# Kernel optimization log

Hardware: AMD Instinct MI355X
Metric: run time of the kernel (lower is better)

The kernel has to match this reference:

```python
import jax, jax.numpy as jnp
import numpy as np

N_NODES = 50000
N_EDGES = 640000
H_DIM = 128


def setup_inputs() -> dict:
    key = jax.random.key(0)
    k1, k2, k3, k4 = jax.random.split(key, 4)
    node_feat = jax.random.normal(k1, (N_NODES, H_DIM), dtype=jnp.float32)
    src = jax.random.randint(k2, (N_EDGES,), 0, N_NODES, dtype=jnp.int64)
    dst = jax.random.randint(k3, (N_EDGES,), 0, N_NODES, dtype=jnp.int64)
    # glorot-uniform kernel, zero bias (as in the original initializers)
    limit = np.sqrt(6.0 / (2 * H_DIM + H_DIM)).astype(np.float32)
    W = jax.random.uniform(k4, (2 * H_DIM, H_DIM), minval=-limit, maxval=limit, dtype=jnp.float32)
    b = jnp.zeros((H_DIM,), dtype=jnp.float32)
    return {"node_feat": node_feat, "src": src, "dst": dst, "W": W, "b": b}


def reference(node_feat, src, dst, W, b):
    # per-edge message: concat(h[src], h[dst]) -> linear  : [E, 2d] @ [2d, d]
    msg = jnp.concatenate([node_feat[src], node_feat[dst]], axis=-1)
    edge_feat = msg @ W + b  # [E, d]
    # scatter-sum over destination nodes (zero for in-degree-0 nodes, as DGL update_all)
    agg = jax.ops.segment_sum(edge_feat, dst, num_segments=node_feat.shape[0])  # [N, d]
    # node apply: sigmoid(aggregated msg) + softplus(old h)
    return jax.nn.sigmoid(agg) + jax.nn.softplus(node_feat)
```

## Files before the change

### kernel.cpp

```cpp
#include <hip/hip_runtime.h>
#include <math.h>

#define HD 128
#define CAP 32
#define OVCAP 8192
#define NPROD 256
#define PBCAP 64
#define BINSZ 512
#define MAXBINS 112
#define NPB 16
#define RPT 8

typedef __attribute__((ext_vector_type(8))) short bf16x8;
typedef __attribute__((ext_vector_type(4))) float f32x4;

__device__ inline short f2bf(float x) {
    union { float f; unsigned u; } v; v.f = x;
    unsigned r = v.u + 0x7fff + ((v.u >> 16) & 1);
    return (short)(r >> 16);
}

#define LOG2E 1.4426950408889634f
#define LN2   0.6931471805599453f

__device__ inline float fast_sigmoid(float x) {
    return __builtin_amdgcn_rcpf(1.0f + __builtin_amdgcn_exp2f(-LOG2E * x));
}
__device__ inline float fast_softplus(float x) {
    float t = __builtin_amdgcn_exp2f(-LOG2E * fabsf(x));
    return fmaxf(x, 0.0f) + LN2 * __builtin_amdgcn_logf(1.0f + t);
}

__device__ inline void accum8(float* a, const uint4 u) {
    a[0] += __uint_as_float(u.x << 16);
    a[1] += __uint_as_float(u.x & 0xffff0000u);
    a[2] += __uint_as_float(u.y << 16);
    a[3] += __uint_as_float(u.y & 0xffff0000u);
    a[4] += __uint_as_float(u.z << 16);
    a[5] += __uint_as_float(u.z & 0xffff0000u);
    a[6] += __uint_as_float(u.w << 16);
    a[7] += __uint_as_float(u.w & 0xffff0000u);
}


__global__ __launch_bounds__(256) void prep0(
    const float* __restrict__ W, short* __restrict__ WtG,
    int* __restrict__ ovA_cnt, int* __restrict__ ovB_cnt)
{
    const int tid = blockIdx.x * 256 + threadIdx.x;
    const int total = gridDim.x * 256;
    if (tid == 0) { *ovA_cnt = 0; *ovB_cnt = 0; }
    for (int i = tid; i < 256 * 128; i += total) {
        int j = i >> 7, k = i & 127;
        float w = (j < HD) ? W[k * HD + j] : W[(HD + k) * HD + (j - HD)];
        WtG[i] = f2bf(w);
    }
}

__global__ __launch_bounds__(256) void partA(
    const int* __restrict__ src, const int* __restrict__ dst,
    unsigned* __restrict__ pb_buf,
    int* __restrict__ pb_cnt,
    unsigned* __restrict__ ovA, int* __restrict__ ovA_cnt,
    int n_edges, int nbins)
{
    __shared__ unsigned buf[MAXBINS][PBCAP];
    __shared__ int bcnt[MAXBINS];

    const int t = threadIdx.x;
    for (int i = t; i < nbins; i += 256) bcnt[i] = 0;
    __syncthreads();

    const int chunk = (n_edges + NPROD - 1) / NPROD;
    int e0 = blockIdx.x * chunk;
    int e1 = e0 + chunk; if (e1 > n_edges) e1 = n_edges;

    for (int e = e0 + t; e < e1; e += 256) {
        int d = dst[e], s = src[e];
        int bin = d >> 9;
        unsigned pk = ((unsigned)d << 16) | (unsigned)s;
        int pos = atomicAdd(&bcnt[bin], 1);
        if (pos < PBCAP) buf[bin][pos] = pk;
        else {
            int op = atomicAdd(ovA_cnt, 1);
            if (op < OVCAP) ovA[op] = pk;
        }
    }
    __syncthreads();

    unsigned* myb = pb_buf + (size_t)blockIdx.x * nbins * PBCAP;
    int* myc = pb_cnt + (size_t)blockIdx.x * nbins;
    for (int b = 0; b < nbins; ++b) {
        int c = bcnt[b]; if (c > PBCAP) c = PBCAP;
        if (t < c) myb[(size_t)b * PBCAP + t] = buf[b][t];
        if (t == 0) myc[b] = c;
    }
}

__global__ __launch_bounds__(256) void partB(
    const unsigned* __restrict__ pb_buf, const int* __restrict__ pb_cnt,
    const unsigned* __restrict__ ovA, const int* __restrict__ ovA_cnt,
    unsigned* __restrict__ ovB, int* __restrict__ ovB_cnt,
    int* __restrict__ cnt, unsigned short* __restrict__ bkt,
    int n_nodes, int nbins)
{
    __shared__ unsigned short lbkt[BINSZ][CAP];
    __shared__ int lcnt[BINSZ];

    const int t = threadIdx.x;
    const int bin = blockIdx.x;
    const int base = bin * BINSZ;

    for (int i = t; i < BINSZ; i += 256) lcnt[i] = 0;
    __syncthreads();

    {
        int c = pb_cnt[(size_t)t * nbins + bin];
        const unsigned* seg = pb_buf + ((size_t)t * nbins + bin) * PBCAP;
        for (int i = 0; i < c; ++i) {
            unsigned e = seg[i];
            int dl = (int)(e >> 16) - base;
            int pos = atomicAdd(&lcnt[dl], 1);
            if (pos < CAP) lbkt[dl][pos] = (unsigned short)(e & 0xffffu);
            else {
                int op = atomicAdd(ovB_cnt, 1);
                if (op < OVCAP) ovB[op] = e;
            }
        }
    }
    {
        int oc = *ovA_cnt; if (oc > OVCAP) oc = OVCAP;
        for (int i = t; i < oc; i += 256) {
            unsigned e = ovA[i];
            int d = (int)(e >> 16);
            if ((d >> 9) == bin) {
                int dl = d - base;
                int pos = atomicAdd(&lcnt[dl], 1);
                if (pos < CAP) lbkt[dl][pos] = (unsigned short)(e & 0xffffu);
                else {
                    int op = atomicAdd(ovB_cnt, 1);
                    if (op < OVCAP) ovB[op] = e;
                }
            }
        }
    }
    __syncthreads();

    for (int g0 = t; g0 < BINSZ; g0 += 256) {
        int g = base + g0;
        if (g < n_nodes) {
            cnt[g] = lcnt[g0];
            uint4* dstp = (uint4*)(bkt + (size_t)g * CAP);
            const uint4* srcp = (const uint4*)&lbkt[g0][0];
            dstp[0] = srcp[0];
            dstp[1] = srcp[1];
            dstp[2] = srcp[2];
            dstp[3] = srcp[3];
        }
    }
}


__global__ __launch_bounds__(256) void prep_gemm(
    const float* __restrict__ h,
    const short* __restrict__ WtG,
    const float* __restrict__ bias,
    short* __restrict__ m1b,
    short* __restrict__ m2b,
    int n_nodes)
{
    __shared__ short sb[2][2][16][72];

    const int lane = threadIdx.x & 63;
    const int wv = threadIdx.x >> 6;
    const int half = wv & 1;
    const int ch = wv >> 1;
    const int c0 = ch * 64;
    const int row = lane & 15;
    const int g = lane >> 4;
    const int mBlk = blockIdx.x * 64;

    bf16x8 B[4][4];
    #pragma unroll
    for (int jt = 0; jt < 4; ++jt) {
        const short* wj = WtG + (size_t)(half * HD + c0 + jt * 16 + row) * HD + g * 8;
        #pragma unroll
        for (int kf = 0; kf < 4; ++kf)
            B[jt][kf] = *(const bf16x8*)(wj + kf * 32);
    }
    float bc[4];
    #pragma unroll
    for (int jt = 0; jt < 4; ++jt) bc[jt] = half ? bias[c0 + jt * 16 + row] : 0.f;

    short* const dstp = half ? m2b : m1b;

    float4 af[8];
    {
        int mA = mBlk + row; if (mA > n_nodes - 1) mA = n_nodes - 1;
        #pragma unroll
        for (int kf = 0; kf < 4; ++kf) {
            af[2 * kf]     = *(const float4*)(h + (size_t)mA * HD + kf * 32 + g * 8);
            af[2 * kf + 1] = *(const float4*)(h + (size_t)mA * HD + kf * 32 + g * 8 + 4);
        }
    }

    #pragma unroll
    for (int tt = 0; tt < 4; ++tt) {
        const int m0 = mBlk + tt * 16;

        bf16x8 a[4];
        #pragma unroll
        for (int kf = 0; kf < 4; ++kf) {
            float4 x = af[2 * kf], y = af[2 * kf + 1];
            bf16x8 t = { f2bf(x.x), f2bf(x.y), f2bf(x.z), f2bf(x.w),
                         f2bf(y.x), f2bf(y.y), f2bf(y.z), f2bf(y.w) };
            a[kf] = t;
        }
        if (tt < 3) {
            int mN = m0 + 16 + row; if (mN > n_nodes - 1) mN = n_nodes - 1;
            #pragma unroll
            for (int kf = 0; kf < 4; ++kf) {
                af[2 * kf]     = *(const float4*)(h + (size_t)mN * HD + kf * 32 + g * 8);
                af[2 * kf + 1] = *(const float4*)(h + (size_t)mN * HD + kf * 32 + g * 8 + 4);
            }
        }

        f32x4 acc[4];
        #pragma unroll
        for (int jt = 0; jt < 4; ++jt) acc[jt] = (f32x4){0.f, 0.f, 0.f, 0.f};
        #pragma unroll
        for (int jt = 0; jt < 4; ++jt)
            #pragma unroll
            for (int kf = 0; kf < 4; ++kf)
                acc[jt] = __builtin_amdgcn_mfma_f32_16x16x32_bf16(a[kf], B[jt][kf], acc[jt], 0, 0, 0);

        #pragma unroll
        for (int jt = 0; jt < 4; ++jt)
            #pragma unroll
            for (int r = 0; r < 4; ++r)
                sb[half][ch][g * 4 + r][jt * 16 + row] = f2bf(acc[jt][r] + bc[jt]);
        asm volatile("s_waitcnt lgkmcnt(0)" ::: "memory");
        #pragma unroll
        for (int ps = 0; ps < 2; ++ps) {
            int rr = ps * 8 + (lane >> 3);
            int c8 = lane & 7;
            int n = m0 + rr;
            bf16x8 v = *(const bf16x8*)&sb[half][ch][rr][c8 * 8];
            if (n < n_nodes)
                *(bf16x8*)(dstp + (size_t)n * HD + c0 + c8 * 8) = v;
        }
    }
}


__global__ __launch_bounds__(256) void gather_ep(
    const short* __restrict__ m1b, const int* __restrict__ cnt,
    const unsigned short* __restrict__ bkt,
    const unsigned* __restrict__ ov, const int* __restrict__ ov_cnt,
    const short* __restrict__ m2b,
    const float* __restrict__ h, float* __restrict__ out, int n_nodes)
{
    int g = (blockIdx.x * 256 + threadIdx.x) >> 4;
    int lane = threadIdx.x & 15;
    if (g >= n_nodes) return;
    const int degree = cnt[g];
    const int end = (degree < CAP) ? degree : CAP;
    const unsigned short* bl = bkt + (size_t)g * CAP;
    const size_t lo = (size_t)(lane * 8);

    float a0[8], a1[8];
    #pragma unroll
    for (int q = 0; q < 8; ++q) { a0[q] = 0.f; a1[q] = 0.f; }

    if (end > 0) {
        const int lastv = bl[end - 1];
        const uint4* bl4 = (const uint4*)bl;
        for (int base = 0; base < end; base += 8) {
            uint4 iv = bl4[base >> 3];
            int id8[8];
            id8[0] = iv.x & 0xffff; id8[1] = iv.x >> 16;
            id8[2] = iv.y & 0xffff; id8[3] = iv.y >> 16;
            id8[4] = iv.z & 0xffff; id8[5] = iv.z >> 16;
            id8[6] = iv.w & 0xffff; id8[7] = iv.w >> 16;
            #pragma unroll
            for (int j = 0; j < 8; ++j)
                if (base + j >= end) id8[j] = lastv;
            uint4 v[8];
            #pragma unroll
            for (int j = 0; j < 8; ++j)
                v[j] = *(const uint4*)(m1b + (size_t)id8[j] * HD + lo);
            #pragma unroll
            for (int j = 0; j < 8; ++j) {
                if (base + j < end) accum8((j & 1) ? a1 : a0, v[j]);
            }
        }
    }

    if (degree > CAP) {
        int oc = *ov_cnt; if (oc > OVCAP) oc = OVCAP;
        for (int i = 0; i < oc; ++i) {
            unsigned v = ov[i];
            if ((int)(v >> 16) == g) {
                uint4 vv = *(const uint4*)(m1b + (size_t)(v & 0xffffu) * HD + lo);
                accum8(a0, vv);
            }
        }
    }

    const float dg = (float)degree;
    uint4 mv = *(const uint4*)(m2b + (size_t)g * HD + lo);
    float mr[8];
    mr[0] = __uint_as_float(mv.x << 16); mr[1] = __uint_as_float(mv.x & 0xffff0000u);
    mr[2] = __uint_as_float(mv.y << 16); mr[3] = __uint_as_float(mv.y & 0xffff0000u);
    mr[4] = __uint_as_float(mv.z << 16); mr[5] = __uint_as_float(mv.z & 0xffff0000u);
    mr[6] = __uint_as_float(mv.w << 16); mr[7] = __uint_as_float(mv.w & 0xffff0000u);

    const float4* ph = (const float4*)(h + (size_t)g * HD + lo);
    float4 ha = ph[0], hb4 = ph[1];
    float hr[8] = { ha.x, ha.y, ha.z, ha.w, hb4.x, hb4.y, hb4.z, hb4.w };

    float o[8];
    #pragma unroll
    for (int q = 0; q < 8; ++q) {
        float agg = (a0[q] + a1[q]) + dg * mr[q];
        o[q] = fast_sigmoid(agg) + fast_softplus(hr[q]);
    }
    float4* po = (float4*)(out + (size_t)g * HD + lo);
    po[0] = (float4){o[0], o[1], o[2], o[3]};
    po[1] = (float4){o[4], o[5], o[6], o[7]};
}


__global__ __launch_bounds__(256) void zero_i32(int* __restrict__ p, int n)
{
    int i = blockIdx.x * 256 + threadIdx.x;
    if (i < n) p[i] = 0;
}

__global__ __launch_bounds__(256) void wt_convert(
    const float* __restrict__ W, short* __restrict__ Wt)
{
    int idx = blockIdx.x * 256 + threadIdx.x;
    int j = idx >> 8;
    int k = idx & 255;
    Wt[idx] = f2bf(W[k * HD + j]);
}

__global__ __launch_bounds__(256) void mpnn_scatter(
    const float* __restrict__ h, const int* __restrict__ src,
    const int* __restrict__ dst, float* __restrict__ S,
    int* __restrict__ deg, int n_edges)
{
    int gid = blockIdx.x * 256 + threadIdx.x;
    int e = gid >> 5;
    if (e >= n_edges) return;
    int lane = gid & 31;
    int s = src[e], d = dst[e];
    float4 v = *(const float4*)(h + (size_t)s * HD + lane * 4);
    float* srow = S + (size_t)d * HD + lane * 4;
    atomicAdd(srow + 0, v.x);
    atomicAdd(srow + 1, v.y);
    atomicAdd(srow + 2, v.z);
    atomicAdd(srow + 3, v.w);
    if (lane == 0) atomicAdd(deg + d, 1);
}

__global__ __launch_bounds__(256) void mpnn_node_mfma(
    const float* __restrict__ h,
    const short* __restrict__ Wt,
    const float* __restrict__ bias,
    const int* __restrict__ deg,
    float* __restrict__ S,
    int n_nodes)
{
    const int lane = threadIdx.x & 63;
    const int wv = threadIdx.x >> 6;
    const int m0 = blockIdx.x * 32 + (wv >> 1) * 16;
    const int c0 = (wv & 1) * 64;
    if (m0 >= n_nodes) return;
    const int row = lane & 15;
    const int g = lane >> 4;

    const int nBase = m0 + g * 4;
    float dgO[4], hv[4][4], bc[4];
    #pragma unroll
    for (int r = 0; r < 4; ++r) {
        int n = nBase + r;
        int nc = (n < n_nodes) ? n : (n_nodes - 1);
        dgO[r] = (float)deg[nc];
        #pragma unroll
        for (int jt = 0; jt < 4; ++jt)
            hv[jt][r] = h[(size_t)nc * HD + c0 + jt * 16 + row];
    }
    #pragma unroll
    for (int jt = 0; jt < 4; ++jt) bc[jt] = bias[c0 + jt * 16 + row];

    int mA = m0 + row;
    if (mA > n_nodes - 1) mA = n_nodes - 1;
    const float dgA = (float)deg[mA];

    bf16x8 a[8];
    #pragma unroll
    for (int kf = 0; kf < 4; ++kf) {
        const float4* p = (const float4*)(S + (size_t)mA * HD + kf * 32 + g * 8);
        float4 x = p[0], y = p[1];
        bf16x8 t = { f2bf(x.x), f2bf(x.y), f2bf(x.z), f2bf(x.w),
                     f2bf(y.x), f2bf(y.y), f2bf(y.z), f2bf(y.w) };
        a[kf] = t;
    }
    #pragma unroll
    for (int kf = 0; kf < 4; ++kf) {
        const float4* p = (const float4*)(h + (size_t)mA * HD + kf * 32 + g * 8);
        float4 x = p[0], y = p[1];
        bf16x8 t = { f2bf(dgA * x.x), f2bf(dgA * x.y), f2bf(dgA * x.z), f2bf(dgA * x.w),
                     f2bf(dgA * y.x), f2bf(dgA * y.y), f2bf(dgA * y.z), f2bf(dgA * y.w) };
        a[4 + kf] = t;
    }

    f32x4 acc[4];
    #pragma unroll
    for (int jt = 0; jt < 4; ++jt) acc[jt] = (f32x4){0.f, 0.f, 0.f, 0.f};

    #pragma unroll
    for (int jt = 0; jt < 4; ++jt) {
        const short* wj = Wt + (size_t)(c0 + jt * 16 + row) * 256 + g * 8;
        #pragma unroll
        for (int kf = 0; kf < 8; ++kf) {
            bf16x8 bf = *(const bf16x8*)(wj + kf * 32);
            acc[jt] = __builtin_amdgcn_mfma_f32_16x16x32_bf16(a[kf], bf, acc[jt], 0, 0, 0);
        }
    }

    #pragma unroll
    for (int jt = 0; jt < 4; ++jt) {
        const int col = c0 + jt * 16 + row;
        #pragma unroll
        for (int r = 0; r < 4; ++r) {
            int n = nBase + r;
            if (n < n_nodes) {
                float agg = acc[jt][r] + dgO[r] * bc[jt];
                S[(size_t)n * HD + col] = fast_sigmoid(agg) + fast_softplus(hv[jt][r]);
            }
        }
    }
}

__global__ __launch_bounds__(256) void mpnn_node_f32(
    const float* __restrict__ h, const float* __restrict__ W,
    const float* __restrict__ b, const int* __restrict__ deg,
    float* __restrict__ S, int n_nodes)
{
    const int j = threadIdx.x & (HD - 1);
    const int g = threadIdx.x >> 7;
    const int n0 = blockIdx.x * NPB + g * RPT;

    float accS[RPT], accH[RPT];
    #pragma unroll
    for (int r = 0; r < RPT; ++r) { accS[r] = 0.f; accH[r] = 0.f; }

    int rmax = n_nodes - n0;
    if (rmax > RPT) rmax = RPT;
    if (rmax < 0) rmax = 0;

    for (int k = 0; k < HD; k += 4) {
        float w0 = W[(k + 0) * HD + j], w1 = W[(k + 1) * HD + j];
        float w2 = W[(k + 2) * HD + j], w3 = W[(k + 3) * HD + j];
        #pragma unroll
        for (int r = 0; r < RPT; ++r) if (r < rmax) {
            float4 a = *(const float4*)(S + (size_t)(n0 + r) * HD + k);
            accS[r] = fmaf(a.x, w0, fmaf(a.y, w1, fmaf(a.z, w2, fmaf(a.w, w3, accS[r]))));
        }
    }
    for (int k = 0; k < HD; k += 4) {
        float w0 = W[(HD + k + 0) * HD + j], w1 = W[(HD + k + 1) * HD + j];
        float w2 = W[(HD + k + 2) * HD + j], w3 = W[(HD + k + 3) * HD + j];
        #pragma unroll
        for (int r = 0; r < RPT; ++r) if (r < rmax) {
            float4 a = *(const float4*)(h + (size_t)(n0 + r) * HD + k);
            accH[r] = fmaf(a.x, w0, fmaf(a.y, w1, fmaf(a.z, w2, fmaf(a.w, w3, accH[r]))));
        }
    }
    __syncthreads();
    #pragma unroll
    for (int r = 0; r < RPT; ++r) if (r < rmax) {
        int n = n0 + r;
        float dg = (float)deg[n];
        float agg = accS[r] + dg * (accH[r] + b[j]);
        float hvv = h[(size_t)n * HD + j];
        S[(size_t)n * HD + j] = fast_sigmoid(agg) + fast_softplus(hvv);
    }
}

extern "C" void kernel_launch(void* const* d_in, const int* in_sizes, int n_in,
                              void* d_out, int out_size, void* d_ws, size_t ws_size,
                              hipStream_t stream)
{
    const float* h   = (const float*)d_in[0];
    const int*   src = (const int*)d_in[1];
    const int*   dst = (const int*)d_in[2];
    const float* W   = (const float*)d_in[3];
    const float* b   = (const float*)d_in[4];
    float* S = (float*)d_out;

    const int n_nodes = in_sizes[0] / HD;
    const int n_edges = in_sizes[1];
    const int WT_INTS = 2 * HD * HD / 2;
    const int nbins = (n_nodes + BINSZ - 1) / BINSZ;

    char* p = (char*)d_ws;
    auto align16 = [](char* q) { return (char*)(((uintptr_t)q + 15) & ~(uintptr_t)15); };
    p = align16(p); int* cnt = (int*)p;                p += (size_t)n_nodes * 4;
    p = align16(p); unsigned short* bkt = (unsigned short*)p; p += (size_t)n_nodes * CAP * 2;
    p = align16(p); short* WtG = (short*)p;            p += (size_t)256 * HD * 2;
    p = align16(p); unsigned* pb_buf = (unsigned*)p;   p += (size_t)NPROD * nbins * PBCAP * 4;
    p = align16(p); int* pb_cnt = (int*)p;             p += (size_t)NPROD * nbins * 4;
    p = align16(p); unsigned* ovA = (unsigned*)p;      p += (size_t)OVCAP * 4;
    p = align16(p); unsigned* ovB = (unsigned*)p;      p += (size_t)OVCAP * 4;
    p = align16(p); int* ovA_cnt = (int*)p;            p += 16;
    p = align16(p); int* ovB_cnt = (int*)p;            p += 16;
    p = align16(p); short* m1b = (short*)p;            p += (size_t)n_nodes * HD * 2;
    p = align16(p); short* m2b = (short*)p;            p += (size_t)n_nodes * HD * 2;
    const size_t need_top = (size_t)(p - (char*)d_ws);

    const size_t need_mid = ((size_t)n_nodes + WT_INTS + 8) * sizeof(int);

    if (n_nodes <= BINSZ * MAXBINS && n_nodes <= 65535 && ws_size >= need_top) {
        prep0<<<128, 256, 0, stream>>>(W, WtG, ovA_cnt, ovB_cnt);

        partA<<<NPROD, 256, 0, stream>>>(src, dst, pb_buf, pb_cnt,
                                         ovA, ovA_cnt, n_edges, nbins);
        partB<<<nbins, 256, 0, stream>>>(pb_buf, pb_cnt, ovA, ovA_cnt,
                                         ovB, ovB_cnt, cnt, bkt, n_nodes, nbins);

        const int pblocks = (n_nodes + 63) / 64;
        prep_gemm<<<pblocks, 256, 0, stream>>>(h, WtG, b, m1b, m2b, n_nodes);

        const int gblocks = (int)(((long long)n_nodes * 16 + 255) / 256);
        gather_ep<<<gblocks, 256, 0, stream>>>(m1b, cnt, bkt, ovB, ovB_cnt,
                                               m2b, h, S, n_nodes);
    } else if (ws_size >= need_mid) {
        int* deg2  = (int*)d_ws;
        short* Wt2 = (short*)(deg2 + n_nodes);
        hipMemsetAsync(d_out, 0, (size_t)n_nodes * HD * sizeof(float), stream);
        zero_i32<<<(n_nodes + 255) / 256, 256, 0, stream>>>(deg2, n_nodes);
        wt_convert<<<(2 * HD * HD) / 256, 256, 0, stream>>>(W, Wt2);
        const int sblocks = (int)(((long long)n_edges * 32 + 255) / 256);
        mpnn_scatter<<<sblocks, 256, 0, stream>>>(h, src, dst, S, deg2, n_edges);
        const int mblocks = (n_nodes + 31) / 32;
        mpnn_node_mfma<<<mblocks, 256, 0, stream>>>(h, Wt2, b, deg2, S, n_nodes);
    } else {
        int* deg2 = (int*)d_ws;
        hipMemsetAsync(d_out, 0, (size_t)n_nodes * HD * sizeof(float), stream);
        zero_i32<<<(n_nodes + 255) / 256, 256, 0, stream>>>(deg2, n_nodes);
        const int sblocks = (int)(((long long)n_edges * 32 + 255) / 256);
        mpnn_scatter<<<sblocks, 256, 0, stream>>>(h, src, dst, S, deg2, n_edges);
        const int nblocks = (n_nodes + NPB - 1) / NPB;
        mpnn_node_f32<<<nblocks, 256, 0, stream>>>(h, W, b, deg2, S, n_nodes);
    }
}
```

Before: 99.48 us.

## Merge bucket partition with node GEMM, parallelize flush, widen gather to 64 lanes per node

The second partition pass and the per-node bf16 GEMM now run in a single launch, with block ranges split by role and shared memory reused through a union. This removes one kernel launch and lets the two independent phases overlap. The partA flush and the partB read loops are flattened so all threads work across every bin slot, replacing the serial per-thread loops. The gather kernel now assigns a full 64-lane wavefront per node, each lane handling two columns with 4-byte loads, instead of 16 lanes with 16-byte loads. This raises parallelism but spends four times as many threads on each node and uses narrower memory accesses.

```diff
diff --git a/kernel.cpp b/kernel.cpp
--- a/kernel.cpp
+++ b/kernel.cpp
@@ -90,95 +90,101 @@
 
     unsigned* myb = pb_buf + (size_t)blockIdx.x * nbins * PBCAP;
     int* myc = pb_cnt + (size_t)blockIdx.x * nbins;
-    for (int b = 0; b < nbins; ++b) {
-        int c = bcnt[b]; if (c > PBCAP) c = PBCAP;
-        if (t < c) myb[(size_t)b * PBCAP + t] = buf[b][t];
-        if (t == 0) myc[b] = c;
-    }
-}
-
-__global__ __launch_bounds__(256) void partB(
+    for (int i = t; i < nbins; i += 256) {
+        int c = bcnt[i]; if (c > PBCAP) c = PBCAP;
+        myc[i] = c;
+    }
+    const int tot = nbins * PBCAP;
+    for (int idx = t; idx < tot; idx += 256) {
+        int b = idx >> 6;
+        int i = idx & 63;
+        if (i < bcnt[b] && i < PBCAP) myb[idx] = buf[b][i];
+    }
+}
+
+
+__global__ __launch_bounds__(256) void partB_gemm(
     const unsigned* __restrict__ pb_buf, const int* __restrict__ pb_cnt,
     const unsigned* __restrict__ ovA, const int* __restrict__ ovA_cnt,
     unsigned* __restrict__ ovB, int* __restrict__ ovB_cnt,
     int* __restrict__ cnt, unsigned short* __restrict__ bkt,
+    const float* __restrict__ h, const short* __restrict__ WtG,
+    const float* __restrict__ bias,
+    short* __restrict__ m1b, short* __restrict__ m2b,
     int n_nodes, int nbins)
 {
-    __shared__ unsigned short lbkt[BINSZ][CAP];
-    __shared__ int lcnt[BINSZ];
+    __shared__ union {
+        struct { unsigned short lbkt[BINSZ][CAP]; int lcnt[BINSZ]; } pb;
+        short sb[2][2][16][72];
+    } u;
 
     const int t = threadIdx.x;
-    const int bin = blockIdx.x;
-    const int base = bin * BINSZ;
-
-    for (int i = t; i < BINSZ; i += 256) lcnt[i] = 0;
-    __syncthreads();
-
-    {
-        int c = pb_cnt[(size_t)t * nbins + bin];
-        const unsigned* seg = pb_buf + ((size_t)t * nbins + bin) * PBCAP;
-        for (int i = 0; i < c; ++i) {
-            unsigned e = seg[i];
-            int dl = (int)(e >> 16) - base;
-            int pos = atomicAdd(&lcnt[dl], 1);
-            if (pos < CAP) lbkt[dl][pos] = (unsigned short)(e & 0xffffu);
-            else {
-                int op = atomicAdd(ovB_cnt, 1);
-                if (op < OVCAP) ovB[op] = e;
-            }
-        }
-    }
-    {
-        int oc = *ovA_cnt; if (oc > OVCAP) oc = OVCAP;
-        for (int i = t; i < oc; i += 256) {
-            unsigned e = ovA[i];
-            int d = (int)(e >> 16);
-            if ((d >> 9) == bin) {
-                int dl = d - base;
-                int pos = atomicAdd(&lcnt[dl], 1);
-                if (pos < CAP) lbkt[dl][pos] = (unsigned short)(e & 0xffffu);
+
+    if ((int)blockIdx.x < nbins) {
+        const int bin = blockIdx.x;
+        const int base = bin * BINSZ;
+
+        for (int i = t; i < BINSZ; i += 256) u.pb.lcnt[i] = 0;
+        __syncthreads();
+
+        const int tot = NPROD * PBCAP;
+        for (int idx = t; idx < tot; idx += 256) {
+            int p = idx >> 6;
+            int i = idx & 63;
+            if (i < pb_cnt[(size_t)p * nbins + bin]) {
+                unsigned e = pb_buf[((size_t)p * nbins + bin) * PBCAP + i];
+                int dl = (int)(e >> 16) - base;
+                int pos = atomicAdd(&u.pb.lcnt[dl], 1);
+                if (pos < CAP) u.pb.lbkt[dl][pos] = (unsigned short)(e & 0xffffu);
                 else {
                     int op = atomicAdd(ovB_cnt, 1);
                     if (op < OVCAP) ovB[op] = e;
                 }
             }
         }
-    }
-    __syncthreads();
-
-    for (int g0 = t; g0 < BINSZ; g0 += 256) {
-        int g = base + g0;
-        if (g < n_nodes) {
-            cnt[g] = lcnt[g0];
-            uint4* dstp = (uint4*)(bkt + (size_t)g * CAP);
-            const uint4* srcp = (const uint4*)&lbkt[g0][0];
-            dstp[0] = srcp[0];
-            dstp[1] = srcp[1];
-            dstp[2] = srcp[2];
-            dstp[3] = srcp[3];
-        }
-    }
-}
-
-
-__global__ __launch_bounds__(256) void prep_gemm(
-    const float* __restrict__ h,
-    const short* __restrict__ WtG,
-    const float* __restrict__ bias,
-    short* __restrict__ m1b,
-    short* __restrict__ m2b,
-    int n_nodes)
-{
-    __shared__ short sb[2][2][16][72];
-
-    const int lane = threadIdx.x & 63;
-    const int wv = threadIdx.x >> 6;
+        {
+            int oc = *ovA_cnt; if (oc > OVCAP) oc = OVCAP;
+            for (int i = t; i < oc; i += 256) {
+                unsigned e = ovA[i];
+                int d = (int)(e >> 16);
+                if ((d >> 9) == bin) {
+                    int dl = d - base;
+                    int pos = atomicAdd(&u.pb.lcnt[dl], 1);
+                    if (pos < CAP) u.pb.lbkt[dl][pos] = (unsigned short)(e & 0xffffu);
+                    else {
+                        int op = atomicAdd(ovB_cnt, 1);
+                        if (op < OVCAP) ovB[op] = e;
+                    }
+                }
+            }
+        }
+        __syncthreads();
+
+        for (int g0 = t; g0 < BINSZ; g0 += 256) {
+            int g = base + g0;
+            if (g < n_nodes) {
+                cnt[g] = u.pb.lcnt[g0];
+                uint4* dstp = (uint4*)(bkt + (size_t)g * CAP);
+                const uint4* srcp = (const uint4*)&u.pb.lbkt[g0][0];
+                dstp[0] = srcp[0];
+                dstp[1] = srcp[1];
+                dstp[2] = srcp[2];
+                dstp[3] = srcp[3];
+            }
+        }
+        return;
+    }
+
+    const int gb = blockIdx.x - nbins;
+    const int lane = t & 63;
+    const int wv = t >> 6;
     const int half = wv & 1;
     const int ch = wv >> 1;
     const int c0 = ch * 64;
     const int row = lane & 15;
     const int g = lane >> 4;
-    const int mBlk = blockIdx.x * 64;
+    const int mBlk = gb * 64;
+    if (mBlk >= n_nodes) return;
 
     bf16x8 B[4][4];
     #pragma unroll
@@ -212,9 +218,9 @@
         #pragma unroll
         for (int kf = 0; kf < 4; ++kf) {
             float4 x = af[2 * kf], y = af[2 * kf + 1];
-            bf16x8 t = { f2bf(x.x), f2bf(x.y), f2bf(x.z), f2bf(x.w),
-                         f2bf(y.x), f2bf(y.y), f2bf(y.z), f2bf(y.w) };
-            a[kf] = t;
+            bf16x8 tr = { f2bf(x.x), f2bf(x.y), f2bf(x.z), f2bf(x.w),
+                          f2bf(y.x), f2bf(y.y), f2bf(y.z), f2bf(y.w) };
+            a[kf] = tr;
         }
         if (tt < 3) {
             int mN = m0 + 16 + row; if (mN > n_nodes - 1) mN = n_nodes - 1;
@@ -238,14 +244,14 @@
         for (int jt = 0; jt < 4; ++jt)
             #pragma unroll
             for (int r = 0; r < 4; ++r)
-                sb[half][ch][g * 4 + r][jt * 16 + row] = f2bf(acc[jt][r] + bc[jt]);
+                u.sb[half][ch][g * 4 + r][jt * 16 + row] = f2bf(acc[jt][r] + bc[jt]);
         asm volatile("s_waitcnt lgkmcnt(0)" ::: "memory");
         #pragma unroll
         for (int ps = 0; ps < 2; ++ps) {
             int rr = ps * 8 + (lane >> 3);
             int c8 = lane & 7;
             int n = m0 + rr;
-            bf16x8 v = *(const bf16x8*)&sb[half][ch][rr][c8 * 8];
+            bf16x8 v = *(const bf16x8*)&u.sb[half][ch][rr][c8 * 8];
             if (n < n_nodes)
                 *(bf16x8*)(dstp + (size_t)n * HD + c0 + c8 * 8) = v;
         }
@@ -260,17 +266,15 @@
     const short* __restrict__ m2b,
     const float* __restrict__ h, float* __restrict__ out, int n_nodes)
 {
-    int g = (blockIdx.x * 256 + threadIdx.x) >> 4;
-    int lane = threadIdx.x & 15;
+    const int g = (blockIdx.x * 256 + threadIdx.x) >> 6;
+    const int lane = threadIdx.x & 63;
     if (g >= n_nodes) return;
     const int degree = cnt[g];
     const int end = (degree < CAP) ? degree : CAP;
     const unsigned short* bl = bkt + (size_t)g * CAP;
-    const size_t lo = (size_t)(lane * 8);
-
-    float a0[8], a1[8];
-    #pragma unroll
-    for (int q = 0; q < 8; ++q) { a0[q] = 0.f; a1[q] = 0.f; }
+    const int co = lane * 2;
+
+    float a0 = 0.f, a1 = 0.f, b0 = 0.f, b1 = 0.f;
 
     if (end > 0) {
         const int lastv = bl[end - 1];
@@ -285,13 +289,18 @@
             #pragma unroll
             for (int j = 0; j < 8; ++j)
                 if (base + j >= end) id8[j] = lastv;
-            uint4 v[8];
+            unsigned v[8];
             #pragma unroll
             for (int j = 0; j < 8; ++j)
-                v[j] = *(const uint4*)(m1b + (size_t)id8[j] * HD + lo);
+                v[j] = *(const unsigned*)(m1b + (size_t)id8[j] * HD + co);
             #pragma unroll
             for (int j = 0; j < 8; ++j) {
-                if (base + j < end) accum8((j & 1) ? a1 : a0, v[j]);
+                if (base + j < end) {
+                    float lo = __uint_as_float(v[j] << 16);
+                    float hi = __uint_as_float(v[j] & 0xffff0000u);
+                    if (j & 1) { b0 += lo; b1 += hi; }
+                    else       { a0 += lo; a1 += hi; }
+                }
             }
         }
     }
@@ -299,35 +308,24 @@
     if (degree > CAP) {
         int oc = *ov_cnt; if (oc > OVCAP) oc = OVCAP;
         for (int i = 0; i < oc; ++i) {
-            unsigned v = ov[i];
-            if ((int)(v >> 16) == g) {
-                uint4 vv = *(const uint4*)(m1b + (size_t)(v & 0xffffu) * HD + lo);
-                accum8(a0, vv);
+            unsigned e = ov[i];
+            if ((int)(e >> 16) == g) {
+                unsigned vv = *(const unsigned*)(m1b + (size_t)(e & 0xffffu) * HD + co);
+                a0 += __uint_as_float(vv << 16);
+                a1 += __uint_as_float(vv & 0xffff0000u);
             }
         }
     }
 
     const float dg = (float)degree;
-    uint4 mv = *(const uint4*)(m2b + (size_t)g * HD + lo);
-    float mr[8];
-    mr[0] = __uint_as_float(mv.x << 16); mr[1] = __uint_as_float(mv.x & 0xffff0000u);
-    mr[2] = __uint_as_float(mv.y << 16); mr[3] = __uint_as_float(mv.y & 0xffff0000u);
-    mr[4] = __uint_as_float(mv.z << 16); mr[5] = __uint_as_float(mv.z & 0xffff0000u);
-    mr[6] = __uint_as_float(mv.w << 16); mr[7] = __uint_as_float(mv.w & 0xffff0000u);
-
-    const float4* ph = (const float4*)(h + (size_t)g * HD + lo);
-    float4 ha = ph[0], hb4 = ph[1];
-    float hr[8] = { ha.x, ha.y, ha.z, ha.w, hb4.x, hb4.y, hb4.z, hb4.w };
-
-    float o[8];
-    #pragma unroll
-    for (int q = 0; q < 8; ++q) {
-        float agg = (a0[q] + a1[q]) + dg * mr[q];
-        o[q] = fast_sigmoid(agg) + fast_softplus(hr[q]);
-    }
-    float4* po = (float4*)(out + (size_t)g * HD + lo);
-    po[0] = (float4){o[0], o[1], o[2], o[3]};
-    po[1] = (float4){o[4], o[5], o[6], o[7]};
+    unsigned mv = *(const unsigned*)(m2b + (size_t)g * HD + co);
+    float m0 = __uint_as_float(mv << 16);
+    float m1v = __uint_as_float(mv & 0xffff0000u);
+    float2 hv = *(const float2*)(h + (size_t)g * HD + co);
+
+    float o0 = fast_sigmoid((a0 + b0) + dg * m0)  + fast_softplus(hv.x);
+    float o1 = fast_sigmoid((a1 + b1) + dg * m1v) + fast_softplus(hv.y);
+    *(float2*)(out + (size_t)g * HD + co) = (float2){o0, o1};
 }
 
 
@@ -529,13 +527,13 @@
 
         partA<<<NPROD, 256, 0, stream>>>(src, dst, pb_buf, pb_cnt,
                                          ovA, ovA_cnt, n_edges, nbins);
-        partB<<<nbins, 256, 0, stream>>>(pb_buf, pb_cnt, ovA, ovA_cnt,
-                                         ovB, ovB_cnt, cnt, bkt, n_nodes, nbins);
 
         const int pblocks = (n_nodes + 63) / 64;
-        prep_gemm<<<pblocks, 256, 0, stream>>>(h, WtG, b, m1b, m2b, n_nodes);
-
-        const int gblocks = (int)(((long long)n_nodes * 16 + 255) / 256);
+        partB_gemm<<<nbins + pblocks, 256, 0, stream>>>(
+            pb_buf, pb_cnt, ovA, ovA_cnt, ovB, ovB_cnt, cnt, bkt,
+            h, WtG, b, m1b, m2b, n_nodes, nbins);
+
+        const int gblocks = (int)(((long long)n_nodes * 64 + 255) / 256);
         gather_ep<<<gblocks, 256, 0, stream>>>(m1b, cnt, bkt, ovB, ovB_cnt,
                                                m2b, h, S, n_nodes);
     } else if (ws_size >= need_mid) {
```

Measured after the change: 110.2 us. 10.8% more time.
